# Optimization experiments

Hardware: AMD Instinct MI355X
Metric: run time of the kernel (lower is better)

The kernel has to match this reference:

```python
import jax, jax.numpy as jnp
import numpy as np

N_NODES = 100000
N_EDGES = 3200000
LEAKY_SLOPE = 0.01  # torch nn.LeakyReLU default


def setup_inputs() -> dict:
    key = jax.random.key(0)
    ks = jax.random.split(key, 9)
    x = jax.random.normal(ks[0], (N_NODES, 128), dtype=jnp.float32)
    edge_index = jax.random.randint(ks[1], (2, N_EDGES), 0, N_NODES, dtype=jnp.int64)
    weights = jax.random.uniform(ks[2], (N_EDGES,), dtype=jnp.float32)
    # GCNConv linear weights (glorot-ish init) and biases
    def lin(k, fin, fout):
        s = (6.0 / (fin + fout)) ** 0.5
        return jax.random.uniform(k, (fout, fin), dtype=jnp.float32, minval=-s, maxval=s)
    W1 = lin(ks[3], 128, 64); b1 = jnp.zeros((64,), jnp.float32)
    W2 = lin(ks[4], 64, 32);  b2 = jnp.zeros((32,), jnp.float32)
    W3 = lin(ks[5], 32, 4);   b3 = jnp.zeros((4,), jnp.float32)
    return {"x_embeddings": x, "edge_index": edge_index, "weights": weights,
            "W1": W1, "b1": b1, "W2": W2, "b2": b2, "W3": W3, "b3": b3}


def _gcn_norm(src, dst, weights, n_nodes):
    # PyG gcn_norm with add_self_loops=True, fill_value=1
    loop = jnp.arange(n_nodes, dtype=src.dtype)
    src_a = jnp.concatenate([src, loop])
    dst_a = jnp.concatenate([dst, loop])
    w_a = jnp.concatenate([weights, jnp.ones((n_nodes,), weights.dtype)])
    deg = jax.ops.segment_sum(w_a, dst_a, num_segments=n_nodes)
    dis = jnp.where(deg > 0, jax.lax.rsqrt(jnp.where(deg > 0, deg, 1.0)), 0.0)
    norm = dis[src_a] * w_a * dis[dst_a]
    return src_a, dst_a, norm


def _gcn_conv(x, W, b, src_a, dst_a, norm, n_nodes):
    h = x @ W.T                              # [N, fout]
    msg = norm[:, None] * h[src_a]           # [E+N, fout] gather
    out = jax.ops.segment_sum(msg, dst_a, num_segments=n_nodes)  # scatter-add
    return out + b


def reference(x_embeddings, edge_index, weights, W1, b1, W2, b2, W3, b3):
    n = x_embeddings.shape[0]
    src, dst = edge_index[0], edge_index[1]
    src_a, dst_a, norm = _gcn_norm(src, dst, weights, n)
    # eval mode: F.dropout(training=False) is identity
    h = _gcn_conv(x_embeddings, W1, b1, src_a, dst_a, norm, n)
    h = jax.nn.leaky_relu(h, LEAKY_SLOPE)
    h = _gcn_conv(h, W2, b2, src_a, dst_a, norm, n)
    h = jax.nn.leaky_relu(h, LEAKY_SLOPE)
    h = _gcn_conv(h, W3, b3, src_a, dst_a, norm, n)
    return jax.nn.softmax(h, axis=1)
```

## Files before the change

kernel.cpp:

```cpp
#include <hip/hip_runtime.h>
#include <hip/hip_fp16.h>


#define BLK 256

typedef _Float16 f16x8 __attribute__((ext_vector_type(8)));
typedef float f32x4 __attribute__((ext_vector_type(4)));

__global__ __launch_bounds__(256) void k_hist(const int* __restrict__ dst,
                                              int* __restrict__ hist,
                                              int E, int CH, int NB) {
    __shared__ int h[256];
    int b = blockIdx.x, t = threadIdx.x;
    h[t] = 0;
    __syncthreads();
    int beg = b * CH, fin = min(E, beg + CH);
    for (int e = beg + t; e < fin; e += 256)
        atomicAdd(&h[dst[e] >> 9], 1);
    __syncthreads();
    if (t < NB) hist[t * 256 + b] = h[t];
}

__global__ void k_scan1(const int* __restrict__ in, int* __restrict__ outv,
                        int* __restrict__ partials, int n) {
    __shared__ int sm[256];
    int i = blockIdx.x * 256 + threadIdx.x;
    int v = (i < n) ? in[i] : 0;
    sm[threadIdx.x] = v;
    __syncthreads();
    for (int off = 1; off < 256; off <<= 1) {
        int t = (threadIdx.x >= off) ? sm[threadIdx.x - off] : 0;
        __syncthreads();
        sm[threadIdx.x] += t;
        __syncthreads();
    }
    if (i < n) outv[i] = sm[threadIdx.x] - v;
    if (threadIdx.x == 255) partials[blockIdx.x] = sm[255];
}

__global__ void k_scan2(int* __restrict__ partials, int nb) {
    __shared__ int sm[512];
    int t = threadIdx.x;
    int v = (t < nb) ? partials[t] : 0;
    sm[t] = v;
    __syncthreads();
    for (int off = 1; off < 512; off <<= 1) {
        int x = (t >= off) ? sm[t - off] : 0;
        __syncthreads();
        sm[t] += x;
        __syncthreads();
    }
    if (t < nb) partials[t] = sm[t] - v;
}

__global__ void k_scan3(int* __restrict__ data, const int* __restrict__ partials, int n) {
    int i = blockIdx.x * 256 + threadIdx.x;
    if (i < n) data[i] += partials[i >> 8];
}

__global__ __launch_bounds__(256) void k_bscatter(const int* __restrict__ src,
                                                  const int* __restrict__ dst,
                                                  const float* __restrict__ w,
                                                  const int* __restrict__ scanout,
                                                  int2* __restrict__ tmp,
                                                  int E, int CH, int NB) {
    __shared__ int cur[256];
    int b = blockIdx.x, t = threadIdx.x;
    if (t < NB) cur[t] = scanout[t * 256 + b];
    __syncthreads();
    int beg = b * CH, fin = min(E, beg + CH);
    for (int e = beg + t; e < fin; e += 256) {
        int d = dst[e];
        int q = d >> 9;
        int pos = atomicAdd(&cur[q], 1);
        tmp[pos] = make_int2(((d & 511) << 18) | src[e], __float_as_int(w[e]));
    }
}

__global__ __launch_bounds__(256) void k_bcsr(const int* __restrict__ scanout,
                                              const int2* __restrict__ tmp,
                                              int2* __restrict__ pack,
                                              int* __restrict__ row_ptr,
                                              float* __restrict__ dis,
                                              int n, int E, int NB) {
    __shared__ int cnt[512];
    __shared__ float wsum[512];
    __shared__ int psum[256];
    int q = blockIdx.x, t = threadIdx.x;
    int base = scanout[q * 256];
    int end  = (q == NB - 1) ? E : scanout[(q + 1) * 256];
    cnt[t] = 0; cnt[t + 256] = 0;
    wsum[t] = 0.f; wsum[t + 256] = 0.f;
    __syncthreads();
    for (int j = base + t; j < end; j += 256) {
        int2 r = tmp[j];
        int d = r.x >> 18;
        atomicAdd(&cnt[d], 1);
        atomicAdd(&wsum[d], __int_as_float(r.y));
    }
    __syncthreads();
    int a = cnt[2 * t], bb = cnt[2 * t + 1];
    psum[t] = a + bb;
    __syncthreads();
    for (int off = 1; off < 256; off <<= 1) {
        int v = (t >= off) ? psum[t - off] : 0;
        __syncthreads();
        psum[t] += v;
        __syncthreads();
    }
    int pex = psum[t] - (a + bb);
    __syncthreads();
    cnt[2 * t] = pex;
    cnt[2 * t + 1] = pex + a;
    int node0 = q * 512;
    if (node0 + 2 * t < n) {
        row_ptr[node0 + 2 * t] = base + pex;
        dis[node0 + 2 * t] = rsqrtf(1.f + wsum[2 * t]);
    }
    if (node0 + 2 * t + 1 < n) {
        row_ptr[node0 + 2 * t + 1] = base + pex + a;
        dis[node0 + 2 * t + 1] = rsqrtf(1.f + wsum[2 * t + 1]);
    }
    if (q == 0 && t == 0) row_ptr[n] = E;
    __syncthreads();
    for (int j = base + t; j < end; j += 256) {
        int2 r = tmp[j];
        int d = r.x >> 18;
        int pos = base + atomicAdd(&cnt[d], 1);
        pack[pos] = make_int2(r.x & 0x3FFFF, r.y);
    }
}

__global__ __launch_bounds__(256) void k_norm(const int* __restrict__ rp,
                                              const float* __restrict__ dis,
                                              int2* __restrict__ pack, int n) {
    int node = blockIdx.x * 4 + (threadIdx.x >> 6);
    int lane = threadIdx.x & 63;
    if (node >= n) return;
    float dd = dis[node];
    int beg = rp[node], end = rp[node + 1];
    for (int j = beg + lane; j < end; j += 64) {
        int2 p = pack[j];
        p.y = __float_as_int(dd * __int_as_float(p.y) * dis[p.x]);
        pack[j] = p;
    }
}

__device__ __forceinline__ float leaky01(float v) {
    return v > 0.f ? v : 0.01f * v;
}
__device__ __forceinline__ float h2f(ushort u) {
    return __half2float(__ushort_as_half(u));
}
__device__ __forceinline__ ushort f2h(float f) {
    return __half_as_ushort(__float2half(f));
}
__device__ __forceinline__ float2 h2f2(uint u) {
    return make_float2(h2f((ushort)(u & 0xffff)), h2f((ushort)(u >> 16)));
}

__global__ __launch_bounds__(256) void k_linear1(
        const float* __restrict__ in, const float* __restrict__ W,
        ushort* __restrict__ outh, int n) {
    constexpr int WS = 136;
    __shared__ _Float16 sW[64 * WS];
    int tid = threadIdx.x;
    for (int i = tid; i < 8192; i += 256) {
        int c = i >> 7, k = i & 127;
        sW[c * WS + k] = (_Float16)W[i];
    }
    __syncthreads();
    int w = tid >> 6, l = tid & 63;
    int lr = l & 15, lg = l >> 4;
    int row0 = blockIdx.x * 64 + w * 16;
    if (row0 >= n) return;
    int arow = min(row0 + lr, n - 1);
    const float* xr = in + (size_t)arow * 128 + lg * 8;

    f32x4 acc[4] = {{0.f,0.f,0.f,0.f},{0.f,0.f,0.f,0.f},
                    {0.f,0.f,0.f,0.f},{0.f,0.f,0.f,0.f}};
#pragma unroll
    for (int kt = 0; kt < 4; ++kt) {
        float4 a0 = *(const float4*)(xr + kt * 32);
        float4 a1 = *(const float4*)(xr + kt * 32 + 4);
        f16x8 af;
        af[0] = (_Float16)a0.x; af[1] = (_Float16)a0.y;
        af[2] = (_Float16)a0.z; af[3] = (_Float16)a0.w;
        af[4] = (_Float16)a1.x; af[5] = (_Float16)a1.y;
        af[6] = (_Float16)a1.z; af[7] = (_Float16)a1.w;
#pragma unroll
        for (int ct = 0; ct < 4; ++ct) {
            int c = ct * 16 + lr;
            f16x8 bf = *(const f16x8*)&sW[c * WS + kt * 32 + lg * 8];
            acc[ct] = __builtin_amdgcn_mfma_f32_16x16x32_f16(af, bf, acc[ct], 0, 0, 0);
        }
    }
#pragma unroll
    for (int ct = 0; ct < 4; ++ct) {
#pragma unroll
        for (int i = 0; i < 4; ++i) {
            int r = row0 + lg * 4 + i;
            if (r < n) outh[(size_t)r * 64 + ct * 16 + lr] = f2h(acc[ct][i]);
        }
    }
}

__global__ __launch_bounds__(256) void fgather64(
        const int* __restrict__ rp, const int2* __restrict__ pack,
        const float* __restrict__ dis, const ushort* __restrict__ h1h,
        const float* __restrict__ b1, const float* __restrict__ W2,
        ushort* __restrict__ h2h, int n) {
    __shared__ float sW2t[64 * 33];
    __shared__ float sact[4][64];
    int tid = threadIdx.x;
    for (int i = tid; i < 2048; i += 256)
        sW2t[(i & 63) * 33 + (i >> 6)] = W2[i];
    int w = tid >> 6, l = tid & 63;
    int es = l >> 3, g = l & 7;
    int node = blockIdx.x * 4 + w;
    bool valid = node < n;
    float acc[8] = {0.f, 0.f, 0.f, 0.f, 0.f, 0.f, 0.f, 0.f};
    if (valid) {
        int beg = rp[node], end = rp[node + 1];
        int j = beg;
        for (; j + 16 <= end; j += 16) {
            int2 pa = pack[j + es];
            int2 pb = pack[j + 8 + es];
            uint4 ua = *(const uint4*)&h1h[(size_t)pa.x * 64 + 8 * g];
            uint4 ub = *(const uint4*)&h1h[(size_t)pb.x * 64 + 8 * g];
            float na = __int_as_float(pa.y), nb2 = __int_as_float(pb.y);
            float2 v;
            v = h2f2(ua.x); acc[0] += na * v.x;  acc[1] += na * v.y;
            v = h2f2(ua.y); acc[2] += na * v.x;  acc[3] += na * v.y;
            v = h2f2(ua.z); acc[4] += na * v.x;  acc[5] += na * v.y;
            v = h2f2(ua.w); acc[6] += na * v.x;  acc[7] += na * v.y;
            v = h2f2(ub.x); acc[0] += nb2 * v.x; acc[1] += nb2 * v.y;
            v = h2f2(ub.y); acc[2] += nb2 * v.x; acc[3] += nb2 * v.y;
            v = h2f2(ub.z); acc[4] += nb2 * v.x; acc[5] += nb2 * v.y;
            v = h2f2(ub.w); acc[6] += nb2 * v.x; acc[7] += nb2 * v.y;
        }
        for (; j < end; j += 8) {
            if (j + es < end) {
                int2 p = pack[j + es];
                uint4 u = *(const uint4*)&h1h[(size_t)p.x * 64 + 8 * g];
                float nm = __int_as_float(p.y);
                float2 v;
                v = h2f2(u.x); acc[0] += nm * v.x; acc[1] += nm * v.y;
                v = h2f2(u.y); acc[2] += nm * v.x; acc[3] += nm * v.y;
                v = h2f2(u.z); acc[4] += nm * v.x; acc[5] += nm * v.y;
                v = h2f2(u.w); acc[6] += nm * v.x; acc[7] += nm * v.y;
            }
        }
#pragma unroll
        for (int u = 0; u < 8; ++u) {
            acc[u] += __shfl_xor(acc[u], 8);
            acc[u] += __shfl_xor(acc[u], 16);
            acc[u] += __shfl_xor(acc[u], 32);
        }
        if (es == 0) {
            float dd = dis[node], d2 = dd * dd;
            uint4 u = *(const uint4*)&h1h[(size_t)node * 64 + 8 * g];
            float2 v;
            v = h2f2(u.x); acc[0] += d2 * v.x; acc[1] += d2 * v.y;
            v = h2f2(u.y); acc[2] += d2 * v.x; acc[3] += d2 * v.y;
            v = h2f2(u.z); acc[4] += d2 * v.x; acc[5] += d2 * v.y;
            v = h2f2(u.w); acc[6] += d2 * v.x; acc[7] += d2 * v.y;
#pragma unroll
            for (int u2 = 0; u2 < 8; ++u2)
                sact[w][8 * g + u2] = leaky01(acc[u2] + b1[8 * g + u2]);
        }
    }
    __syncthreads();
    if (valid) {
        int c2 = l & 31, half = l >> 5;
        float s = 0.f;
#pragma unroll 8
        for (int cc = 0; cc < 32; ++cc) {
            int c = half * 32 + cc;
            s += sW2t[c * 33 + c2] * sact[w][c];
        }
        s += __shfl_xor(s, 32);
        if (l < 32) h2h[(size_t)node * 32 + c2] = f2h(s);
    }
}

__global__ __launch_bounds__(256) void fgather32(
        const int* __restrict__ rp, const int2* __restrict__ pack,
        const float* __restrict__ dis, const ushort* __restrict__ h2h,
        const float* __restrict__ b2, const float* __restrict__ W3,
        float* __restrict__ h3out, int n) {
    __shared__ float sW3t[32 * 5];
    __shared__ float sact[4][32];
    int tid = threadIdx.x;
    if (tid < 128) sW3t[(tid & 31) * 5 + (tid >> 5)] = W3[tid];
    int w = tid >> 6, l = tid & 63;
    int es = l >> 3, g = l & 7;
    int node = blockIdx.x * 4 + w;
    bool valid = node < n;
    float acc[4] = {0.f, 0.f, 0.f, 0.f};
    if (valid) {
        int beg = rp[node], end = rp[node + 1];
        int j = beg;
        for (; j + 16 <= end; j += 16) {
            int2 pa = pack[j + es];
            int2 pb = pack[j + 8 + es];
            uint2 ua = *(const uint2*)&h2h[(size_t)pa.x * 32 + 4 * g];
            uint2 ub = *(const uint2*)&h2h[(size_t)pb.x * 32 + 4 * g];
            float na = __int_as_float(pa.y), nb2 = __int_as_float(pb.y);
            float2 v;
            v = h2f2(ua.x); acc[0] += na * v.x;  acc[1] += na * v.y;
            v = h2f2(ua.y); acc[2] += na * v.x;  acc[3] += na * v.y;
            v = h2f2(ub.x); acc[0] += nb2 * v.x; acc[1] += nb2 * v.y;
            v = h2f2(ub.y); acc[2] += nb2 * v.x; acc[3] += nb2 * v.y;
        }
        for (; j < end; j += 8) {
            if (j + es < end) {
                int2 p = pack[j + es];
                uint2 u = *(const uint2*)&h2h[(size_t)p.x * 32 + 4 * g];
                float nm = __int_as_float(p.y);
                float2 v;
                v = h2f2(u.x); acc[0] += nm * v.x; acc[1] += nm * v.y;
                v = h2f2(u.y); acc[2] += nm * v.x; acc[3] += nm * v.y;
            }
        }
#pragma unroll
        for (int u = 0; u < 4; ++u) {
            acc[u] += __shfl_xor(acc[u], 8);
            acc[u] += __shfl_xor(acc[u], 16);
            acc[u] += __shfl_xor(acc[u], 32);
        }
        if (es == 0) {
            float dd = dis[node], d2 = dd * dd;
            uint2 u = *(const uint2*)&h2h[(size_t)node * 32 + 4 * g];
            float2 v;
            v = h2f2(u.x); acc[0] += d2 * v.x; acc[1] += d2 * v.y;
            v = h2f2(u.y); acc[2] += d2 * v.x; acc[3] += d2 * v.y;
#pragma unroll
            for (int u2 = 0; u2 < 4; ++u2)
                sact[w][4 * g + u2] = leaky01(acc[u2] + b2[4 * g + u2]);
        }
    }
    __syncthreads();
    if (valid && l < 32) {
        int c3 = l & 3;
        float s = 0.f;
#pragma unroll
        for (int m = 0; m < 4; ++m) {
            int c = (l >> 2) + 8 * m;
            s += sW3t[c * 5 + c3] * sact[w][c];
        }
        s += __shfl_xor(s, 4, 32);
        s += __shfl_xor(s, 8, 32);
        s += __shfl_xor(s, 16, 32);
        if (l < 4) h3out[(size_t)node * 4 + l] = s;
    }
}

__global__ __launch_bounds__(256) void fgather4(
        const int* __restrict__ rp, const int2* __restrict__ pack,
        const float* __restrict__ dis, const float* __restrict__ h3,
        const float* __restrict__ b3, float* __restrict__ out, int n) {
    int tid = threadIdx.x;
    int node = blockIdx.x * 8 + (tid >> 5);
    int l32 = tid & 31;
    if (node >= n) return;
    int beg = rp[node], end = rp[node + 1];
    float4 acc = make_float4(0.f, 0.f, 0.f, 0.f);
    for (int j = beg + l32; j < end; j += 32) {
        int2 p = pack[j];
        float4 hr = *(const float4*)&h3[(size_t)p.x * 4];
        float nm = __int_as_float(p.y);
        acc.x += nm * hr.x; acc.y += nm * hr.y;
        acc.z += nm * hr.z; acc.w += nm * hr.w;
    }
#pragma unroll
    for (int off = 1; off <= 16; off <<= 1) {
        acc.x += __shfl_xor(acc.x, off, 32);
        acc.y += __shfl_xor(acc.y, off, 32);
        acc.z += __shfl_xor(acc.z, off, 32);
        acc.w += __shfl_xor(acc.w, off, 32);
    }
    if (l32 == 0) {
        float dd = dis[node], d2 = dd * dd;
        float4 hr = *(const float4*)&h3[(size_t)node * 4];
        float v0 = acc.x + d2 * hr.x + b3[0];
        float v1 = acc.y + d2 * hr.y + b3[1];
        float v2 = acc.z + d2 * hr.z + b3[2];
        float v3 = acc.w + d2 * hr.w + b3[3];
        float m = fmaxf(fmaxf(v0, v1), fmaxf(v2, v3));
        float e0 = expf(v0 - m), e1 = expf(v1 - m);
        float e2 = expf(v2 - m), e3 = expf(v3 - m);
        float inv = 1.f / (e0 + e1 + e2 + e3);
        *(float4*)&out[(size_t)node * 4] =
            make_float4(e0 * inv, e1 * inv, e2 * inv, e3 * inv);
    }
}

static inline int cdiv(long long a, int b) { return (int)((a + b - 1) / b); }

extern "C" void kernel_launch(void* const* d_in, const int* in_sizes, int n_in,
                              void* d_out, int out_size, void* d_ws, size_t ws_size,
                              hipStream_t stream) {
    const float* x   = (const float*)d_in[0];
    const int*   ei  = (const int*)d_in[1];
    const float* ew  = (const float*)d_in[2];
    const float* W1  = (const float*)d_in[3];
    const float* b1  = (const float*)d_in[4];
    const float* W2  = (const float*)d_in[5];
    const float* b2  = (const float*)d_in[6];
    const float* W3  = (const float*)d_in[7];
    const float* b3  = (const float*)d_in[8];
    float* out = (float*)d_out;

    const int N = in_sizes[0] / 128;
    const int E = in_sizes[2];
    const int* src = ei;
    const int* dst = ei + E;

    const int NB = (N + 511) >> 9;
    const int GB = 256;
    const int CH = cdiv(E, GB);
    const int n_scan = NB * GB;

    char* base = (char*)d_ws;
    auto alloc = [&](size_t bytes) {
        char* p = base;
        base += (bytes + 255) & ~(size_t)255;
        return p;
    };
    float* dis      = (float*)alloc((size_t)N * 4);
    int*   row_ptr  = (int*)  alloc(((size_t)N + 1) * 4);
    int*   hist     = (int*)  alloc((size_t)n_scan * 4);
    int*   scanout  = (int*)  alloc((size_t)n_scan * 4);
    int*   partials = (int*)  alloc(512 * 4);
    int2*  pack     = (int2*) alloc((size_t)E * 8);
    char*  regA     = alloc((size_t)N * 64 * 4);
    char*  regB     = alloc((size_t)N * 64 * 4);
    int2*   tmp = (int2*)regA;
    ushort* h1h = (ushort*)regA;
    float*  h3  = (float*)regA;
    ushort* h2h = (ushort*)regB;

    k_hist<<<GB, 256, 0, stream>>>(dst, hist, E, CH, NB);
    k_scan1<<<cdiv(n_scan, 256), 256, 0, stream>>>(hist, scanout, partials, n_scan);
    k_scan2<<<1, 512, 0, stream>>>(partials, cdiv(n_scan, 256));
    k_scan3<<<cdiv(n_scan, 256), 256, 0, stream>>>(scanout, partials, n_scan);
    k_bscatter<<<GB, 256, 0, stream>>>(src, dst, ew, scanout, tmp, E, CH, NB);
    k_bcsr<<<NB, 256, 0, stream>>>(scanout, tmp, pack, row_ptr, dis, N, E, NB);
    k_norm<<<cdiv(N, 4), 256, 0, stream>>>(row_ptr, dis, pack, N);

    k_linear1<<<cdiv(N, 64), 256, 0, stream>>>(x, W1, h1h, N);
    fgather64<<<cdiv(N, 4), 256, 0, stream>>>(row_ptr, pack, dis, h1h, b1, W2, h2h, N);
    fgather32<<<cdiv(N, 4), 256, 0, stream>>>(row_ptr, pack, dis, h2h, b2, W3, h3, N);
    fgather4<<<cdiv(N, 8), 256, 0, stream>>>(row_ptr, pack, dis, h3, b3, out, N);
}
```

Baseline: 312.1 us.

## Merge histogram with first linear layer and fold scan fixup into consumers

The histogram kernel and the first dense layer now run as one launch: the first 256 blocks build the per-chunk dst histogram and the remaining blocks run the MFMA linear layer. To make that possible, h1 moves to the second half of regB so it no longer shares memory with the tmp scatter buffer. The separate scan-fixup kernel is removed and its block partials are added where scanout is read in bscatter and bcsr. The gather loops are also rewritten to explicit fmaf with half2 unpacking. This removes two launches and lets the GEMM overlap the histogram, at the cost of a larger shared-memory footprint for the histogram blocks.

```diff
diff --git a/kernel.cpp b/kernel.cpp
--- a/kernel.cpp
+++ b/kernel.cpp
@@ -7,18 +7,64 @@
 typedef _Float16 f16x8 __attribute__((ext_vector_type(8)));
 typedef float f32x4 __attribute__((ext_vector_type(4)));
 
-__global__ __launch_bounds__(256) void k_hist(const int* __restrict__ dst,
-                                              int* __restrict__ hist,
-                                              int E, int CH, int NB) {
-    __shared__ int h[256];
+__global__ __launch_bounds__(256) void k_hist_lin1(
+        const int* __restrict__ dst, int* __restrict__ hist, int E, int CH, int NB,
+        const float* __restrict__ xin, const float* __restrict__ W1,
+        ushort* __restrict__ outh, int n) {
+    __shared__ __align__(16) char smem[64 * 136 * 2];
     int b = blockIdx.x, t = threadIdx.x;
-    h[t] = 0;
-    __syncthreads();
-    int beg = b * CH, fin = min(E, beg + CH);
-    for (int e = beg + t; e < fin; e += 256)
-        atomicAdd(&h[dst[e] >> 9], 1);
-    __syncthreads();
-    if (t < NB) hist[t * 256 + b] = h[t];
+    if (b < 256) {
+        int* h = (int*)smem;
+        h[t] = 0;
+        __syncthreads();
+        int beg = b * CH, fin = min(E, beg + CH);
+        for (int e = beg + t; e < fin; e += 256)
+            atomicAdd(&h[dst[e] >> 9], 1);
+        __syncthreads();
+        if (t < NB) hist[t * 256 + b] = h[t];
+        return;
+    }
+    _Float16* sW = (_Float16*)smem;
+    constexpr int WS = 136;
+    for (int i = t; i < 8192; i += 256) {
+        int c = i >> 7, k = i & 127;
+        sW[c * WS + k] = (_Float16)W1[i];
+    }
+    __syncthreads();
+    int w = t >> 6, l = t & 63;
+    int lr = l & 15, lg = l >> 4;
+    int row0 = (b - 256) * 64 + w * 16;
+    if (row0 >= n) return;
+    int arow = min(row0 + lr, n - 1);
+    const float* xr = xin + (size_t)arow * 128 + lg * 8;
+
+    f32x4 acc[4] = {{0.f,0.f,0.f,0.f},{0.f,0.f,0.f,0.f},
+                    {0.f,0.f,0.f,0.f},{0.f,0.f,0.f,0.f}};
+#pragma unroll
+    for (int kt = 0; kt < 4; ++kt) {
+        float4 a0 = *(const float4*)(xr + kt * 32);
+        float4 a1 = *(const float4*)(xr + kt * 32 + 4);
+        f16x8 af;
+        af[0] = (_Float16)a0.x; af[1] = (_Float16)a0.y;
+        af[2] = (_Float16)a0.z; af[3] = (_Float16)a0.w;
+        af[4] = (_Float16)a1.x; af[5] = (_Float16)a1.y;
+        af[6] = (_Float16)a1.z; af[7] = (_Float16)a1.w;
+#pragma unroll
+        for (int ct = 0; ct < 4; ++ct) {
+            int c = ct * 16 + lr;
+            f16x8 bf = *(const f16x8*)&sW[c * WS + kt * 32 + lg * 8];
+            acc[ct] = __builtin_amdgcn_mfma_f32_16x16x32_f16(af, bf, acc[ct], 0, 0, 0);
+        }
+    }
+#pragma unroll
+    for (int ct = 0; ct < 4; ++ct) {
+#pragma unroll
+        for (int i = 0; i < 4; ++i) {
+            int r = row0 + lg * 4 + i;
+            if (r < n) outh[(size_t)r * 64 + ct * 16 + lr] =
+                __half_as_ushort(__float2half(acc[ct][i]));
+        }
+    }
 }
 
 __global__ void k_scan1(const int* __restrict__ in, int* __restrict__ outv,
@@ -53,20 +99,16 @@
     if (t < nb) partials[t] = sm[t] - v;
 }
 
-__global__ void k_scan3(int* __restrict__ data, const int* __restrict__ partials, int n) {
-    int i = blockIdx.x * 256 + threadIdx.x;
-    if (i < n) data[i] += partials[i >> 8];
-}
-
 __global__ __launch_bounds__(256) void k_bscatter(const int* __restrict__ src,
                                                   const int* __restrict__ dst,
                                                   const float* __restrict__ w,
                                                   const int* __restrict__ scanout,
+                                                  const int* __restrict__ partials,
                                                   int2* __restrict__ tmp,
                                                   int E, int CH, int NB) {
     __shared__ int cur[256];
     int b = blockIdx.x, t = threadIdx.x;
-    if (t < NB) cur[t] = scanout[t * 256 + b];
+    if (t < NB) cur[t] = scanout[t * 256 + b] + partials[t];
     __syncthreads();
     int beg = b * CH, fin = min(E, beg + CH);
     for (int e = beg + t; e < fin; e += 256) {
@@ -78,6 +120,7 @@
 }
 
 __global__ __launch_bounds__(256) void k_bcsr(const int* __restrict__ scanout,
+                                              const int* __restrict__ partials,
                                               const int2* __restrict__ tmp,
                                               int2* __restrict__ pack,
                                               int* __restrict__ row_ptr,
@@ -87,8 +130,8 @@
     __shared__ float wsum[512];
     __shared__ int psum[256];
     int q = blockIdx.x, t = threadIdx.x;
-    int base = scanout[q * 256];
-    int end  = (q == NB - 1) ? E : scanout[(q + 1) * 256];
+    int base = scanout[q * 256] + partials[q];
+    int end  = (q == NB - 1) ? E : (scanout[(q + 1) * 256] + partials[q + 1]);
     cnt[t] = 0; cnt[t + 256] = 0;
     wsum[t] = 0.f; wsum[t + 256] = 0.f;
     __syncthreads();
@@ -149,60 +192,11 @@
 __device__ __forceinline__ float leaky01(float v) {
     return v > 0.f ? v : 0.01f * v;
 }
-__device__ __forceinline__ float h2f(ushort u) {
-    return __half2float(__ushort_as_half(u));
-}
 __device__ __forceinline__ ushort f2h(float f) {
     return __half_as_ushort(__float2half(f));
 }
-__device__ __forceinline__ float2 h2f2(uint u) {
-    return make_float2(h2f((ushort)(u & 0xffff)), h2f((ushort)(u >> 16)));
-}
-
-__global__ __launch_bounds__(256) void k_linear1(
-        const float* __restrict__ in, const float* __restrict__ W,
-        ushort* __restrict__ outh, int n) {
-    constexpr int WS = 136;
-    __shared__ _Float16 sW[64 * WS];
-    int tid = threadIdx.x;
-    for (int i = tid; i < 8192; i += 256) {
-        int c = i >> 7, k = i & 127;
-        sW[c * WS + k] = (_Float16)W[i];
-    }
-    __syncthreads();
-    int w = tid >> 6, l = tid & 63;
-    int lr = l & 15, lg = l >> 4;
-    int row0 = blockIdx.x * 64 + w * 16;
-    if (row0 >= n) return;
-    int arow = min(row0 + lr, n - 1);
-    const float* xr = in + (size_t)arow * 128 + lg * 8;
-
-    f32x4 acc[4] = {{0.f,0.f,0.f,0.f},{0.f,0.f,0.f,0.f},
-                    {0.f,0.f,0.f,0.f},{0.f,0.f,0.f,0.f}};
-#pragma unroll
-    for (int kt = 0; kt < 4; ++kt) {
-        float4 a0 = *(const float4*)(xr + kt * 32);
-        float4 a1 = *(const float4*)(xr + kt * 32 + 4);
-        f16x8 af;
-        af[0] = (_Float16)a0.x; af[1] = (_Float16)a0.y;
-        af[2] = (_Float16)a0.z; af[3] = (_Float16)a0.w;
-        af[4] = (_Float16)a1.x; af[5] = (_Float16)a1.y;
-        af[6] = (_Float16)a1.z; af[7] = (_Float16)a1.w;
-#pragma unroll
-        for (int ct = 0; ct < 4; ++ct) {
-            int c = ct * 16 + lr;
-            f16x8 bf = *(const f16x8*)&sW[c * WS + kt * 32 + lg * 8];
-            acc[ct] = __builtin_amdgcn_mfma_f32_16x16x32_f16(af, bf, acc[ct], 0, 0, 0);
-        }
-    }
-#pragma unroll
-    for (int ct = 0; ct < 4; ++ct) {
-#pragma unroll
-        for (int i = 0; i < 4; ++i) {
-            int r = row0 + lg * 4 + i;
-            if (r < n) outh[(size_t)r * 64 + ct * 16 + lr] = f2h(acc[ct][i]);
-        }
-    }
+__device__ __forceinline__ __half2 bch2(uint v) {
+    union { uint u; __half2 h; } c; c.u = v; return c.h;
 }
 
 __global__ __launch_bounds__(256) void fgather64(
@@ -229,26 +223,38 @@
             uint4 ua = *(const uint4*)&h1h[(size_t)pa.x * 64 + 8 * g];
             uint4 ub = *(const uint4*)&h1h[(size_t)pb.x * 64 + 8 * g];
             float na = __int_as_float(pa.y), nb2 = __int_as_float(pb.y);
-            float2 v;
-            v = h2f2(ua.x); acc[0] += na * v.x;  acc[1] += na * v.y;
-            v = h2f2(ua.y); acc[2] += na * v.x;  acc[3] += na * v.y;
-            v = h2f2(ua.z); acc[4] += na * v.x;  acc[5] += na * v.y;
-            v = h2f2(ua.w); acc[6] += na * v.x;  acc[7] += na * v.y;
-            v = h2f2(ub.x); acc[0] += nb2 * v.x; acc[1] += nb2 * v.y;
-            v = h2f2(ub.y); acc[2] += nb2 * v.x; acc[3] += nb2 * v.y;
-            v = h2f2(ub.z); acc[4] += nb2 * v.x; acc[5] += nb2 * v.y;
-            v = h2f2(ub.w); acc[6] += nb2 * v.x; acc[7] += nb2 * v.y;
+            __half2 h0;
+            h0 = bch2(ua.x); acc[0] = fmaf(__low2float(h0), na, acc[0]);
+                             acc[1] = fmaf(__high2float(h0), na, acc[1]);
+            h0 = bch2(ua.y); acc[2] = fmaf(__low2float(h0), na, acc[2]);
+                             acc[3] = fmaf(__high2float(h0), na, acc[3]);
+            h0 = bch2(ua.z); acc[4] = fmaf(__low2float(h0), na, acc[4]);
+                             acc[5] = fmaf(__high2float(h0), na, acc[5]);
+            h0 = bch2(ua.w); acc[6] = fmaf(__low2float(h0), na, acc[6]);
+                             acc[7] = fmaf(__high2float(h0), na, acc[7]);
+            h0 = bch2(ub.x); acc[0] = fmaf(__low2float(h0), nb2, acc[0]);
+                             acc[1] = fmaf(__high2float(h0), nb2, acc[1]);
+            h0 = bch2(ub.y); acc[2] = fmaf(__low2float(h0), nb2, acc[2]);
+                             acc[3] = fmaf(__high2float(h0), nb2, acc[3]);
+            h0 = bch2(ub.z); acc[4] = fmaf(__low2float(h0), nb2, acc[4]);
+                             acc[5] = fmaf(__high2float(h0), nb2, acc[5]);
+            h0 = bch2(ub.w); acc[6] = fmaf(__low2float(h0), nb2, acc[6]);
+                             acc[7] = fmaf(__high2float(h0), nb2, acc[7]);
         }
         for (; j < end; j += 8) {
             if (j + es < end) {
                 int2 p = pack[j + es];
                 uint4 u = *(const uint4*)&h1h[(size_t)p.x * 64 + 8 * g];
                 float nm = __int_as_float(p.y);
-                float2 v;
-                v = h2f2(u.x); acc[0] += nm * v.x; acc[1] += nm * v.y;
-                v = h2f2(u.y); acc[2] += nm * v.x; acc[3] += nm * v.y;
-                v = h2f2(u.z); acc[4] += nm * v.x; acc[5] += nm * v.y;
-                v = h2f2(u.w); acc[6] += nm * v.x; acc[7] += nm * v.y;
+                __half2 h0;
+                h0 = bch2(u.x); acc[0] = fmaf(__low2float(h0), nm, acc[0]);
+                                acc[1] = fmaf(__high2float(h0), nm, acc[1]);
+                h0 = bch2(u.y); acc[2] = fmaf(__low2float(h0), nm, acc[2]);
+                                acc[3] = fmaf(__high2float(h0), nm, acc[3]);
+                h0 = bch2(u.z); acc[4] = fmaf(__low2float(h0), nm, acc[4]);
+                                acc[5] = fmaf(__high2float(h0), nm, acc[5]);
+                h0 = bch2(u.w); acc[6] = fmaf(__low2float(h0), nm, acc[6]);
+                                acc[7] = fmaf(__high2float(h0), nm, acc[7]);
             }
         }
 #pragma unroll
@@ -260,11 +266,15 @@
         if (es == 0) {
             float dd = dis[node], d2 = dd * dd;
             uint4 u = *(const uint4*)&h1h[(size_t)node * 64 + 8 * g];
-            float2 v;
-            v = h2f2(u.x); acc[0] += d2 * v.x; acc[1] += d2 * v.y;
-            v = h2f2(u.y); acc[2] += d2 * v.x; acc[3] += d2 * v.y;
-            v = h2f2(u.z); acc[4] += d2 * v.x; acc[5] += d2 * v.y;
-            v = h2f2(u.w); acc[6] += d2 * v.x; acc[7] += d2 * v.y;
+            __half2 h0;
+            h0 = bch2(u.x); acc[0] = fmaf(__low2float(h0), d2, acc[0]);
+                            acc[1] = fmaf(__high2float(h0), d2, acc[1]);
+            h0 = bch2(u.y); acc[2] = fmaf(__low2float(h0), d2, acc[2]);
+                            acc[3] = fmaf(__high2float(h0), d2, acc[3]);
+            h0 = bch2(u.z); acc[4] = fmaf(__low2float(h0), d2, acc[4]);
+                            acc[5] = fmaf(__high2float(h0), d2, acc[5]);
+            h0 = bch2(u.w); acc[6] = fmaf(__low2float(h0), d2, acc[6]);
+                            acc[7] = fmaf(__high2float(h0), d2, acc[7]);
 #pragma unroll
             for (int u2 = 0; u2 < 8; ++u2)
                 sact[w][8 * g + u2] = leaky01(acc[u2] + b1[8 * g + u2]);
@@ -307,20 +317,26 @@
             uint2 ua = *(const uint2*)&h2h[(size_t)pa.x * 32 + 4 * g];
             uint2 ub = *(const uint2*)&h2h[(size_t)pb.x * 32 + 4 * g];
             float na = __int_as_float(pa.y), nb2 = __int_as_float(pb.y);
-            float2 v;
-            v = h2f2(ua.x); acc[0] += na * v.x;  acc[1] += na * v.y;
-            v = h2f2(ua.y); acc[2] += na * v.x;  acc[3] += na * v.y;
-            v = h2f2(ub.x); acc[0] += nb2 * v.x; acc[1] += nb2 * v.y;
-            v = h2f2(ub.y); acc[2] += nb2 * v.x; acc[3] += nb2 * v.y;
+            __half2 h0;
+            h0 = bch2(ua.x); acc[0] = fmaf(__low2float(h0), na, acc[0]);
+                             acc[1] = fmaf(__high2float(h0), na, acc[1]);
+            h0 = bch2(ua.y); acc[2] = fmaf(__low2float(h0), na, acc[2]);
+                             acc[3] = fmaf(__high2float(h0), na, acc[3]);
+            h0 = bch2(ub.x); acc[0] = fmaf(__low2float(h0), nb2, acc[0]);
+                             acc[1] = fmaf(__high2float(h0), nb2, acc[1]);
+            h0 = bch2(ub.y); acc[2] = fmaf(__low2float(h0), nb2, acc[2]);
+                             acc[3] = fmaf(__high2float(h0), nb2, acc[3]);
         }
         for (; j < end; j += 8) {
             if (j + es < end) {
                 int2 p = pack[j + es];
                 uint2 u = *(const uint2*)&h2h[(size_t)p.x * 32 + 4 * g];
                 float nm = __int_as_float(p.y);
-                float2 v;
-                v = h2f2(u.x); acc[0] += nm * v.x; acc[1] += nm * v.y;
-                v = h2f2(u.y); acc[2] += nm * v.x; acc[3] += nm * v.y;
+                __half2 h0;
+                h0 = bch2(u.x); acc[0] = fmaf(__low2float(h0), nm, acc[0]);
+                                acc[1] = fmaf(__high2float(h0), nm, acc[1]);
+                h0 = bch2(u.y); acc[2] = fmaf(__low2float(h0), nm, acc[2]);
+                                acc[3] = fmaf(__high2float(h0), nm, acc[3]);
             }
         }
 #pragma unroll
@@ -332,9 +348,11 @@
         if (es == 0) {
             float dd = dis[node], d2 = dd * dd;
             uint2 u = *(const uint2*)&h2h[(size_t)node * 32 + 4 * g];
-            float2 v;
-            v = h2f2(u.x); acc[0] += d2 * v.x; acc[1] += d2 * v.y;
-            v = h2f2(u.y); acc[2] += d2 * v.x; acc[3] += d2 * v.y;
+            __half2 h0;
+            h0 = bch2(u.x); acc[0] = fmaf(__low2float(h0), d2, acc[0]);
+                            acc[1] = fmaf(__high2float(h0), d2, acc[1]);
+            h0 = bch2(u.y); acc[2] = fmaf(__low2float(h0), d2, acc[2]);
+                            acc[3] = fmaf(__high2float(h0), d2, acc[3]);
 #pragma unroll
             for (int u2 = 0; u2 < 4; ++u2)
                 sact[w][4 * g + u2] = leaky01(acc[u2] + b2[4 * g + u2]);
@@ -437,19 +455,18 @@
     char*  regA     = alloc((size_t)N * 64 * 4);
     char*  regB     = alloc((size_t)N * 64 * 4);
     int2*   tmp = (int2*)regA;
-    ushort* h1h = (ushort*)regA;
     float*  h3  = (float*)regA;
     ushort* h2h = (ushort*)regB;
-
-    k_hist<<<GB, 256, 0, stream>>>(dst, hist, E, CH, NB);
+    ushort* h1h = (ushort*)(regB + (size_t)N * 64 * 2);
+
+    k_hist_lin1<<<256 + cdiv(N, 64), 256, 0, stream>>>(
+        dst, hist, E, CH, NB, x, W1, h1h, N);
     k_scan1<<<cdiv(n_scan, 256), 256, 0, stream>>>(hist, scanout, partials, n_scan);
     k_scan2<<<1, 512, 0, stream>>>(partials, cdiv(n_scan, 256));
-    k_scan3<<<cdiv(n_scan, 256), 256, 0, stream>>>(scanout, partials, n_scan);
-    k_bscatter<<<GB, 256, 0, stream>>>(src, dst, ew, scanout, tmp, E, CH, NB);
-    k_bcsr<<<NB, 256, 0, stream>>>(scanout, tmp, pack, row_ptr, dis, N, E, NB);
+    k_bscatter<<<GB, 256, 0, stream>>>(src, dst, ew, scanout, partials, tmp, E, CH, NB);
+    k_bcsr<<<NB, 256, 0, stream>>>(scanout, partials, tmp, pack, row_ptr, dis, N, E, NB);
     k_norm<<<cdiv(N, 4), 256, 0, stream>>>(row_ptr, dis, pack, N);
 
-    k_linear1<<<cdiv(N, 64), 256, 0, stream>>>(x, W1, h1h, N);
     fgather64<<<cdiv(N, 4), 256, 0, stream>>>(row_ptr, pack, dis, h1h, b1, W2, h2h, N);
     fgather32<<<cdiv(N, 4), 256, 0, stream>>>(row_ptr, pack, dis, h2h, b2, W3, h3, N);
     fgather4<<<cdiv(N, 8), 256, 0, stream>>>(row_ptr, pack, dis, h3, b3, out, N);
```

After: 302.7 us. 3.0% less time.
